# Kernel tuning notes

Measured on AMD Instinct MI355X. Metric: run time of the kernel, lower is better.

The kernel has to match this reference:

```python
import jax, jax.numpy as jnp
from jax import lax
import numpy as np

B, T, F, H = 2048, 256, 64, 32


def setup_inputs() -> dict:
    key = jax.random.key(0)
    k = jax.random.split(key, 7)
    s_ih = 1.0 / np.sqrt(H)  # PyTorch GRU init scale uniform(-1/sqrt(H), 1/sqrt(H))
    return {
        "x": jax.random.normal(k[0], (B, T, F), dtype=jnp.float32),
        "W_ih": jax.random.uniform(k[1], (3 * H, F), minval=-s_ih, maxval=s_ih, dtype=jnp.float32),
        "W_hh": jax.random.uniform(k[2], (3 * H, H), minval=-s_ih, maxval=s_ih, dtype=jnp.float32),
        "b_ih": jax.random.uniform(k[3], (3 * H,), minval=-s_ih, maxval=s_ih, dtype=jnp.float32),
        "b_hh": jax.random.uniform(k[4], (3 * H,), minval=-s_ih, maxval=s_ih, dtype=jnp.float32),
        "W_head": jax.random.uniform(k[5], (1, H), minval=-s_ih, maxval=s_ih, dtype=jnp.float32),
        "b_head": jax.random.uniform(k[6], (1,), minval=-s_ih, maxval=s_ih, dtype=jnp.float32),
    }


def _gru_last_hidden(x, W_ih, W_hh, b_ih, b_hh):
    # Precompute input-to-gate projections for all timesteps: [B,T,3H] -> [T,B,3H]
    xg = jnp.einsum("btf,gf->btg", x, W_ih) + b_ih
    xg = jnp.moveaxis(xg, 1, 0)

    def step(h, xt):
        hg = h @ W_hh.T + b_hh  # [B,3H]
        xr, xz, xn = jnp.split(xt, 3, axis=-1)  # PyTorch gate order: r, z, n
        hr, hz, hn = jnp.split(hg, 3, axis=-1)
        r = jax.nn.sigmoid(xr + hr)
        z = jax.nn.sigmoid(xz + hz)
        n = jnp.tanh(xn + r * hn)
        h_new = (1.0 - z) * n + z * h
        return h_new, None

    h0 = jnp.zeros((x.shape[0], W_hh.shape[1]), dtype=x.dtype)
    hT, _ = lax.scan(step, h0, xg)
    return hT  # [B,H] == out[:, -1, :]


def reference(x, W_ih, W_hh, b_ih, b_hh, W_head, b_head):
    hT = _gru_last_hidden(x, W_ih, W_hh, b_ih, b_hh)
    y = hT @ W_head.T + b_head  # [B,1]
    return jax.nn.sigmoid(y)
```

## Files before the change

kernel.cpp:

```cpp
#include <hip/hip_runtime.h>
#include <cstdint>


#define TSEQ 256
#define CSTRIDE 104

typedef __attribute__((ext_vector_type(8))) short bf16x8;
typedef __attribute__((ext_vector_type(4))) float f32x4;
union BF8 { unsigned u[4]; bf16x8 v; };

__device__ __forceinline__ unsigned bfr(float f) {
    unsigned u = __float_as_uint(f);
    return u + 0x7fffu + ((u >> 16) & 1u);
}
__device__ __forceinline__ unsigned packhi(unsigned a, unsigned b) {
    return __builtin_amdgcn_perm(b, a, 0x07060302u);
}
__device__ __forceinline__ void cvt2(const float4& f0, const float4& f1,
                                     bf16x8& hi, bf16x8& lo) {
    float f[8] = {f0.x,f0.y,f0.z,f0.w, f1.x,f1.y,f1.z,f1.w};
    BF8 H, L;
    #pragma unroll
    for (int d = 0; d < 4; ++d) {
        float a = f[2*d], b = f[2*d+1];
        unsigned ua = __float_as_uint(a), ub = __float_as_uint(b);
        float ra = a - __uint_as_float(ua & 0xffff0000u);
        float rb = b - __uint_as_float(ub & 0xffff0000u);
        H.u[d] = packhi(ua, ub);
        L.u[d] = packhi(bfr(ra), bfr(rb));
    }
    hi = H.v; lo = L.v;
}
__device__ __forceinline__ float sel4(f32x4 v, int u) {
    float a = (u & 1) ? v[1] : v[0];
    float b = (u & 1) ? v[3] : v[2];
    return (u & 2) ? b : a;
}
__device__ __forceinline__ float sigx(float v) {
    return __builtin_amdgcn_rcpf(1.f + exp2f(-1.4426950408889634f * v));
}
__device__ __forceinline__ float tanhx(float v) {
    float e = exp2f(-2.8853900817779268f * fabsf(v));
    return copysignf((1.f - e) * __builtin_amdgcn_rcpf(1.f + e), v);
}

#define MFMA16(A, B, C) __builtin_amdgcn_mfma_f32_16x16x32_bf16((A), (B), (C), 0, 0, 0)

#define QBCAST(x, w) ((unsigned)__builtin_amdgcn_update_dpp( \
        0, (int)(x), ((w) | ((w)<<2) | ((w)<<4) | ((w)<<6)), 0xf, 0xf, true))

__device__ __forceinline__ void barrier_nodrain() {
    asm volatile("s_waitcnt lgkmcnt(0)" ::: "memory");
    __builtin_amdgcn_s_barrier();
    asm volatile("" ::: "memory");
}

__global__ __launch_bounds__(256, 1)
void gru_fused(const float* __restrict__ x, const float* __restrict__ W_ih,
               const float* __restrict__ W_hh, const float* __restrict__ b_ih,
               const float* __restrict__ b_hh, const float* __restrict__ W_head,
               const float* __restrict__ b_head, float* __restrict__ out)
{
    __shared__ float xsh[2][2][16 * CSTRIDE];
    const int tid  = threadIdx.x;
    const int wid  = tid >> 6;
    const int lane = tid & 63;
    const int m = lane & 15, q = lane >> 4;
    const int b0 = blockIdx.x * 8;

    if (wid >= 2) {
        const int pq = wid - 2;
        const int bq = m & 3, u = m >> 2;
        bf16x8 Aih[6][2];
        #pragma unroll
        for (int nt = 0; nt < 6; ++nt)
            #pragma unroll
            for (int c = 0; c < 2; ++c) {
                const float* wp = W_ih + (nt*16 + m)*64 + c*32 + q*8;
                BF8 t;
                #pragma unroll
                for (int d = 0; d < 4; ++d) t.u[d] = packhi(bfr(wp[2*d]), bfr(wp[2*d+1]));
                Aih[nt][c] = t.v;
            }
        float4 ring[4];
        const float* xcol = x + ((size_t)(b0 + pq*4 + bq)*TSEQ + u)*64 + q*8;
        auto ldring = [&](int grp) {
            const float* p = xcol + grp*256;
            ring[0] = ((const float4*)p)[0];        ring[1] = ((const float4*)p)[1];
            ring[2] = ((const float4*)(p+32))[0];   ring[3] = ((const float4*)(p+32))[1];
        };
        auto projwrite = [&](int buf) {
            bf16x8 Xh0, Xl0, Xh1, Xl1;
            cvt2(ring[0], ring[1], Xh0, Xl0);
            cvt2(ring[2], ring[3], Xh1, Xl1);
            #pragma unroll
            for (int nt = 0; nt < 6; ++nt) {
                f32x4 a = MFMA16(Aih[nt][0], Xh0, ((f32x4){0.f,0.f,0.f,0.f}));
                a = MFMA16(Aih[nt][0], Xl0, a);
                a = MFMA16(Aih[nt][1], Xh1, a);
                a = MFMA16(Aih[nt][1], Xl1, a);
                *(f32x4*)&xsh[buf][pq][m*CSTRIDE + nt*16 + q*4] = a;
            }
        };
        ldring(0);
        projwrite(0);
        ldring(1);
        barrier_nodrain();
        for (int g = 0; g < 64; ++g) {
            if (g < 63) {
                projwrite((g + 1) & 1);
                ldring(g + 2 < 64 ? g + 2 : 63);
            }
            barrier_nodrain();
        }
    } else {
        const int cq = wid;
        const int bq = m >> 2, u = m & 3;
        bf16x8 Awh[6];
        #pragma unroll
        for (int nt = 0; nt < 6; ++nt) {
            const float* wp = W_hh + (nt*16 + m)*32;
            BF8 t;
            #pragma unroll
            for (int d = 0; d < 4; ++d) {
                int dd = q*4 + d;
                t.u[d] = packhi(bfr(wp[dd]), bfr(wp[dd + 16]));
            }
            Awh[nt] = t.v;
        }
        f32x4 FRZ[4], BN0, BN1;
        #pragma unroll
        for (int nt = 0; nt < 4; ++nt) {
            f32x4 t;
            #pragma unroll
            for (int r = 0; r < 4; ++r) { int g = nt*16 + q*4 + r; t[r] = b_ih[g] + b_hh[g]; }
            FRZ[nt] = t;
        }
        #pragma unroll
        for (int r = 0; r < 4; ++r) { BN0[r] = b_hh[64+q*4+r]; BN1[r] = b_hh[80+q*4+r]; }
        const float fn0 = b_ih[64 + q*4 + u], fn1 = b_ih[80 + q*4 + u];

        unsigned Hd[4] = {0u, 0u, 0u, 0u};
        float hOL = 0.f, hOH = 0.f;
        barrier_nodrain();

        for (int g = 0; g < 64; ++g) {
            const int cbuf = g & 1;
            float xp[4][6];
            #pragma unroll
            for (int s = 0; s < 4; ++s) {
                const float* rp = &xsh[cbuf][cq][(bq + 4*s)*CSTRIDE + q*4 + u];
                #pragma unroll
                for (int nt = 0; nt < 6; ++nt) xp[s][nt] = rp[nt*16];
            }
            #pragma unroll
            for (int s = 0; s < 4; ++s) {
                BF8 bh; bh.u[0]=Hd[0]; bh.u[1]=Hd[1]; bh.u[2]=Hd[2]; bh.u[3]=Hd[3];
                f32x4 a0 = MFMA16(Awh[0], bh.v, FRZ[0]);
                f32x4 a1 = MFMA16(Awh[1], bh.v, FRZ[1]);
                f32x4 a2 = MFMA16(Awh[2], bh.v, FRZ[2]);
                f32x4 a3 = MFMA16(Awh[3], bh.v, FRZ[3]);
                f32x4 a4 = MFMA16(Awh[4], bh.v, BN0);
                f32x4 a5 = MFMA16(Awh[5], bh.v, BN1);

                float r0 = sigx(xp[s][0] + sel4(a0, u));
                float r1 = sigx(xp[s][1] + sel4(a1, u));
                float z0 = sigx(xp[s][2] + sel4(a2, u));
                float z1 = sigx(xp[s][3] + sel4(a3, u));
                float t0 = tanhx(xp[s][4] + fn0 + r0 * sel4(a4, u));
                float t1 = tanhx(xp[s][5] + fn1 + r1 * sel4(a5, u));
                float hNL = t0 + z0 * (hOL - t0);
                float hNH = t1 + z1 * (hOH - t1);
                hOL = hNL; hOH = hNH;

                unsigned pk = packhi(bfr(hNL), bfr(hNH));
                Hd[0] = QBCAST(pk, 0);
                Hd[1] = QBCAST(pk, 1);
                Hd[2] = QBCAST(pk, 2);
                Hd[3] = QBCAST(pk, 3);
            }
            barrier_nodrain();
        }

        float v = hOL * W_head[q*4 + u] + hOH * W_head[16 + q*4 + u];
        v += __shfl_xor(v, 1, 64);
        v += __shfl_xor(v, 2, 64);
        v += __shfl_xor(v, 16, 64);
        v += __shfl_xor(v, 32, 64);
        if (lane < 16 && (lane & 3) == 0)
            out[b0 + cq*4 + (lane >> 2)] = sigx(v + b_head[0]);
    }
}

extern "C" void kernel_launch(void* const* d_in, const int* in_sizes, int n_in,
                              void* d_out, int out_size, void* d_ws, size_t ws_size,
                              hipStream_t stream)
{
    const float* x      = (const float*)d_in[0];
    const float* W_ih   = (const float*)d_in[1];
    const float* W_hh   = (const float*)d_in[2];
    const float* b_ih   = (const float*)d_in[3];
    const float* b_hh   = (const float*)d_in[4];
    const float* W_head = (const float*)d_in[5];
    const float* b_head = (const float*)d_in[6];
    float* out = (float*)d_out;

    gru_fused<<<256, 256, 0, stream>>>(x, W_ih, W_hh, b_ih, b_hh,
                                       W_head, b_head, out);
}
```

Measured before the change: 239.4 us.

## Merge wave pairs so each wave handles two batch groups with interleaved chains

The block shrinks from four waves to two. One wave now projects inputs for both 4-row batch groups, and one wave runs both recurrence chains, A and B, interleaved in the same loop. The goal is instruction-level parallelism: two independent MFMA/activation dependency chains can hide each other's latency inside one wave, instead of relying on separate waves. The trade-offs are higher register pressure and half as many waves per CU, so less latency hiding comes from wave switching.

```diff
diff --git a/kernel.cpp b/kernel.cpp
--- a/kernel.cpp
+++ b/kernel.cpp
@@ -55,7 +55,7 @@
     asm volatile("" ::: "memory");
 }
 
-__global__ __launch_bounds__(256, 1)
+__global__ __launch_bounds__(128, 1)
 void gru_fused(const float* __restrict__ x, const float* __restrict__ W_ih,
                const float* __restrict__ W_hh, const float* __restrict__ b_ih,
                const float* __restrict__ b_hh, const float* __restrict__ W_head,
@@ -68,8 +68,7 @@
     const int m = lane & 15, q = lane >> 4;
     const int b0 = blockIdx.x * 8;
 
-    if (wid >= 2) {
-        const int pq = wid - 2;
+    if (wid == 1) {
         const int bq = m & 3, u = m >> 2;
         bf16x8 Aih[6][2];
         #pragma unroll
@@ -82,24 +81,38 @@
                 for (int d = 0; d < 4; ++d) t.u[d] = packhi(bfr(wp[2*d]), bfr(wp[2*d+1]));
                 Aih[nt][c] = t.v;
             }
-        float4 ring[4];
-        const float* xcol = x + ((size_t)(b0 + pq*4 + bq)*TSEQ + u)*64 + q*8;
+        float4 ringA[4], ringB[4];
+        const float* xcolA = x + ((size_t)(b0 + bq)*TSEQ + u)*64 + q*8;
+        const float* xcolB = x + ((size_t)(b0 + 4 + bq)*TSEQ + u)*64 + q*8;
         auto ldring = [&](int grp) {
-            const float* p = xcol + grp*256;
-            ring[0] = ((const float4*)p)[0];        ring[1] = ((const float4*)p)[1];
-            ring[2] = ((const float4*)(p+32))[0];   ring[3] = ((const float4*)(p+32))[1];
+            const float* pA = xcolA + grp*256;
+            ringA[0] = ((const float4*)pA)[0];        ringA[1] = ((const float4*)pA)[1];
+            ringA[2] = ((const float4*)(pA+32))[0];   ringA[3] = ((const float4*)(pA+32))[1];
+            const float* pB = xcolB + grp*256;
+            ringB[0] = ((const float4*)pB)[0];        ringB[1] = ((const float4*)pB)[1];
+            ringB[2] = ((const float4*)(pB+32))[0];   ringB[3] = ((const float4*)(pB+32))[1];
         };
         auto projwrite = [&](int buf) {
             bf16x8 Xh0, Xl0, Xh1, Xl1;
-            cvt2(ring[0], ring[1], Xh0, Xl0);
-            cvt2(ring[2], ring[3], Xh1, Xl1);
+            cvt2(ringA[0], ringA[1], Xh0, Xl0);
+            cvt2(ringA[2], ringA[3], Xh1, Xl1);
             #pragma unroll
             for (int nt = 0; nt < 6; ++nt) {
                 f32x4 a = MFMA16(Aih[nt][0], Xh0, ((f32x4){0.f,0.f,0.f,0.f}));
                 a = MFMA16(Aih[nt][0], Xl0, a);
                 a = MFMA16(Aih[nt][1], Xh1, a);
                 a = MFMA16(Aih[nt][1], Xl1, a);
-                *(f32x4*)&xsh[buf][pq][m*CSTRIDE + nt*16 + q*4] = a;
+                *(f32x4*)&xsh[buf][0][m*CSTRIDE + nt*16 + q*4] = a;
+            }
+            cvt2(ringB[0], ringB[1], Xh0, Xl0);
+            cvt2(ringB[2], ringB[3], Xh1, Xl1);
+            #pragma unroll
+            for (int nt = 0; nt < 6; ++nt) {
+                f32x4 a = MFMA16(Aih[nt][0], Xh0, ((f32x4){0.f,0.f,0.f,0.f}));
+                a = MFMA16(Aih[nt][0], Xl0, a);
+                a = MFMA16(Aih[nt][1], Xh1, a);
+                a = MFMA16(Aih[nt][1], Xl1, a);
+                *(f32x4*)&xsh[buf][1][m*CSTRIDE + nt*16 + q*4] = a;
             }
         };
         ldring(0);
@@ -114,7 +127,6 @@
             barrier_nodrain();
         }
     } else {
-        const int cq = wid;
         const int bq = m >> 2, u = m & 3;
         bf16x8 Awh[6];
         #pragma unroll
@@ -140,55 +152,84 @@
         for (int r = 0; r < 4; ++r) { BN0[r] = b_hh[64+q*4+r]; BN1[r] = b_hh[80+q*4+r]; }
         const float fn0 = b_ih[64 + q*4 + u], fn1 = b_ih[80 + q*4 + u];
 
-        unsigned Hd[4] = {0u, 0u, 0u, 0u};
-        float hOL = 0.f, hOH = 0.f;
+        unsigned HdA[4] = {0u,0u,0u,0u}, HdB[4] = {0u,0u,0u,0u};
+        float hAL = 0.f, hAH = 0.f, hBL = 0.f, hBH = 0.f;
         barrier_nodrain();
 
         for (int g = 0; g < 64; ++g) {
             const int cbuf = g & 1;
-            float xp[4][6];
+            float xpA[4][6], xpB[4][6];
             #pragma unroll
             for (int s = 0; s < 4; ++s) {
-                const float* rp = &xsh[cbuf][cq][(bq + 4*s)*CSTRIDE + q*4 + u];
+                const float* rpA = &xsh[cbuf][0][(bq + 4*s)*CSTRIDE + q*4 + u];
+                const float* rpB = &xsh[cbuf][1][(bq + 4*s)*CSTRIDE + q*4 + u];
                 #pragma unroll
-                for (int nt = 0; nt < 6; ++nt) xp[s][nt] = rp[nt*16];
+                for (int nt = 0; nt < 6; ++nt) { xpA[s][nt] = rpA[nt*16]; xpB[s][nt] = rpB[nt*16]; }
             }
             #pragma unroll
             for (int s = 0; s < 4; ++s) {
-                BF8 bh; bh.u[0]=Hd[0]; bh.u[1]=Hd[1]; bh.u[2]=Hd[2]; bh.u[3]=Hd[3];
-                f32x4 a0 = MFMA16(Awh[0], bh.v, FRZ[0]);
-                f32x4 a1 = MFMA16(Awh[1], bh.v, FRZ[1]);
-                f32x4 a2 = MFMA16(Awh[2], bh.v, FRZ[2]);
-                f32x4 a3 = MFMA16(Awh[3], bh.v, FRZ[3]);
-                f32x4 a4 = MFMA16(Awh[4], bh.v, BN0);
-                f32x4 a5 = MFMA16(Awh[5], bh.v, BN1);
-
-                float r0 = sigx(xp[s][0] + sel4(a0, u));
-                float r1 = sigx(xp[s][1] + sel4(a1, u));
-                float z0 = sigx(xp[s][2] + sel4(a2, u));
-                float z1 = sigx(xp[s][3] + sel4(a3, u));
-                float t0 = tanhx(xp[s][4] + fn0 + r0 * sel4(a4, u));
-                float t1 = tanhx(xp[s][5] + fn1 + r1 * sel4(a5, u));
-                float hNL = t0 + z0 * (hOL - t0);
-                float hNH = t1 + z1 * (hOH - t1);
-                hOL = hNL; hOH = hNH;
-
-                unsigned pk = packhi(bfr(hNL), bfr(hNH));
-                Hd[0] = QBCAST(pk, 0);
-                Hd[1] = QBCAST(pk, 1);
-                Hd[2] = QBCAST(pk, 2);
-                Hd[3] = QBCAST(pk, 3);
+                BF8 bhA; bhA.u[0]=HdA[0]; bhA.u[1]=HdA[1]; bhA.u[2]=HdA[2]; bhA.u[3]=HdA[3];
+                f32x4 aA0 = MFMA16(Awh[0], bhA.v, FRZ[0]);
+                f32x4 aA1 = MFMA16(Awh[1], bhA.v, FRZ[1]);
+                f32x4 aA2 = MFMA16(Awh[2], bhA.v, FRZ[2]);
+                f32x4 aA3 = MFMA16(Awh[3], bhA.v, FRZ[3]);
+                f32x4 aA4 = MFMA16(Awh[4], bhA.v, BN0);
+                f32x4 aA5 = MFMA16(Awh[5], bhA.v, BN1);
+                BF8 bhB; bhB.u[0]=HdB[0]; bhB.u[1]=HdB[1]; bhB.u[2]=HdB[2]; bhB.u[3]=HdB[3];
+                f32x4 aB0 = MFMA16(Awh[0], bhB.v, FRZ[0]);
+                f32x4 aB1 = MFMA16(Awh[1], bhB.v, FRZ[1]);
+                f32x4 aB2 = MFMA16(Awh[2], bhB.v, FRZ[2]);
+                f32x4 aB3 = MFMA16(Awh[3], bhB.v, FRZ[3]);
+                f32x4 aB4 = MFMA16(Awh[4], bhB.v, BN0);
+                f32x4 aB5 = MFMA16(Awh[5], bhB.v, BN1);
+
+                {
+                    float r0 = sigx(xpA[s][0] + sel4(aA0, u));
+                    float r1 = sigx(xpA[s][1] + sel4(aA1, u));
+                    float z0 = sigx(xpA[s][2] + sel4(aA2, u));
+                    float z1 = sigx(xpA[s][3] + sel4(aA3, u));
+                    float t0 = tanhx(xpA[s][4] + fn0 + r0 * sel4(aA4, u));
+                    float t1 = tanhx(xpA[s][5] + fn1 + r1 * sel4(aA5, u));
+                    float hNL = t0 + z0 * (hAL - t0);
+                    float hNH = t1 + z1 * (hAH - t1);
+                    hAL = hNL; hAH = hNH;
+                    unsigned pk = packhi(bfr(hNL), bfr(hNH));
+                    HdA[0] = QBCAST(pk, 0);
+                    HdA[1] = QBCAST(pk, 1);
+                    HdA[2] = QBCAST(pk, 2);
+                    HdA[3] = QBCAST(pk, 3);
+                }
+                {
+                    float r0 = sigx(xpB[s][0] + sel4(aB0, u));
+                    float r1 = sigx(xpB[s][1] + sel4(aB1, u));
+                    float z0 = sigx(xpB[s][2] + sel4(aB2, u));
+                    float z1 = sigx(xpB[s][3] + sel4(aB3, u));
+                    float t0 = tanhx(xpB[s][4] + fn0 + r0 * sel4(aB4, u));
+                    float t1 = tanhx(xpB[s][5] + fn1 + r1 * sel4(aB5, u));
+                    float hNL = t0 + z0 * (hBL - t0);
+                    float hNH = t1 + z1 * (hBH - t1);
+                    hBL = hNL; hBH = hNH;
+                    unsigned pk = packhi(bfr(hNL), bfr(hNH));
+                    HdB[0] = QBCAST(pk, 0);
+                    HdB[1] = QBCAST(pk, 1);
+                    HdB[2] = QBCAST(pk, 2);
+                    HdB[3] = QBCAST(pk, 3);
+                }
             }
             barrier_nodrain();
         }
 
-        float v = hOL * W_head[q*4 + u] + hOH * W_head[16 + q*4 + u];
-        v += __shfl_xor(v, 1, 64);
-        v += __shfl_xor(v, 2, 64);
-        v += __shfl_xor(v, 16, 64);
-        v += __shfl_xor(v, 32, 64);
-        if (lane < 16 && (lane & 3) == 0)
-            out[b0 + cq*4 + (lane >> 2)] = sigx(v + b_head[0]);
+        const float w0 = W_head[q*4 + u], w1 = W_head[16 + q*4 + u];
+        float vA = hAL * w0 + hAH * w1;
+        float vB = hBL * w0 + hBH * w1;
+        vA += __shfl_xor(vA, 1, 64);  vB += __shfl_xor(vB, 1, 64);
+        vA += __shfl_xor(vA, 2, 64);  vB += __shfl_xor(vB, 2, 64);
+        vA += __shfl_xor(vA, 16, 64); vB += __shfl_xor(vB, 16, 64);
+        vA += __shfl_xor(vA, 32, 64); vB += __shfl_xor(vB, 32, 64);
+        if (lane < 16 && (lane & 3) == 0) {
+            out[b0 + (lane >> 2)]     = sigx(vA + b_head[0]);
+            out[b0 + 4 + (lane >> 2)] = sigx(vB + b_head[0]);
+        }
     }
 }
 
@@ -205,6 +246,6 @@
     const float* b_head = (const float*)d_in[6];
     float* out = (float*)d_out;
 
-    gru_fused<<<256, 256, 0, stream>>>(x, W_ih, W_hh, b_ih, b_hh,
+    gru_fused<<<256, 128, 0, stream>>>(x, W_ih, W_hh, b_ih, b_hh,
                                        W_head, b_head, out);
 }
```

Result: slower. 300.4 us (+25.5%).

## Replace gate transcendentals with shared-reciprocal rational approximations and fold biases into projection

Applied to the files above, without the earlier changes.

Sigmoid and tanh in the recurrent step are replaced by clamped rational polynomial approximations, with one reciprocal shared across the four sigmoid gates and one across the two tanh gates. Input-side biases are folded into the accumulator init of the input projection MFMAs, so the recurrent MFMAs start from zero. The bf16 packing of the hidden state uses a hardware packed-convert instruction. The aim is to shorten the serial per-timestep latency chain by removing exp and rcp instructions, at the cost of approximation error in the activations and slightly different rounding.

```diff
diff --git a/kernel.cpp b/kernel.cpp
--- a/kernel.cpp
+++ b/kernel.cpp
@@ -36,12 +36,22 @@
     float b = (u & 1) ? v[3] : v[2];
     return (u & 2) ? b : a;
 }
-__device__ __forceinline__ float sigx(float v) {
-    return __builtin_amdgcn_rcpf(1.f + exp2f(-1.4426950408889634f * v));
-}
-__device__ __forceinline__ float tanhx(float v) {
-    float e = exp2f(-2.8853900817779268f * fabsf(v));
-    return copysignf((1.f - e) * __builtin_amdgcn_rcpf(1.f + e), v);
+
+__device__ __forceinline__ void sigr(float x, float& xnum, float& den) {
+    float t = x * x;
+    float n = __builtin_fmaf(__builtin_fmaf(__builtin_fmaf(
+                  2.890625e-8f, t, 4.370629e-5f), t, 8.012821e-3f), t, 0.25f);
+    den     = __builtin_fmaf(__builtin_fmaf(__builtin_fmaf(
+                  3.237500e-6f, t, 1.456879e-3f), t, 0.11538462f), t, 1.0f);
+    xnum = x * n;
+}
+__device__ __forceinline__ void tanr(float x, float& xnum, float& den) {
+    float t = x * x;
+    float n = __builtin_fmaf(__builtin_fmaf(__builtin_fmaf(
+                  7.400300e-6f, t, 2.797203e-3f), t, 0.12820513f), t, 1.0f);
+    den     = __builtin_fmaf(__builtin_fmaf(__builtin_fmaf(
+                  2.071987e-4f, t, 2.331002e-2f), t, 0.46153846f), t, 1.0f);
+    xnum = x * n;
 }
 
 #define MFMA16(A, B, C) __builtin_amdgcn_mfma_f32_16x16x32_bf16((A), (B), (C), 0, 0, 0)
@@ -82,6 +92,17 @@
                 for (int d = 0; d < 4; ++d) t.u[d] = packhi(bfr(wp[2*d]), bfr(wp[2*d+1]));
                 Aih[nt][c] = t.v;
             }
+        f32x4 PC[6];
+        #pragma unroll
+        for (int nt = 0; nt < 6; ++nt) {
+            f32x4 t;
+            #pragma unroll
+            for (int r = 0; r < 4; ++r) {
+                int g = nt*16 + q*4 + r;
+                t[r] = (nt < 4) ? (b_ih[g] + b_hh[g]) : b_ih[g];
+            }
+            PC[nt] = t;
+        }
         float4 ring[4];
         const float* xcol = x + ((size_t)(b0 + pq*4 + bq)*TSEQ + u)*64 + q*8;
         auto ldring = [&](int grp) {
@@ -95,7 +116,7 @@
             cvt2(ring[2], ring[3], Xh1, Xl1);
             #pragma unroll
             for (int nt = 0; nt < 6; ++nt) {
-                f32x4 a = MFMA16(Aih[nt][0], Xh0, ((f32x4){0.f,0.f,0.f,0.f}));
+                f32x4 a = MFMA16(Aih[nt][0], Xh0, PC[nt]);
                 a = MFMA16(Aih[nt][0], Xl0, a);
                 a = MFMA16(Aih[nt][1], Xh1, a);
                 a = MFMA16(Aih[nt][1], Xl1, a);
@@ -128,17 +149,10 @@
             }
             Awh[nt] = t.v;
         }
-        f32x4 FRZ[4], BN0, BN1;
-        #pragma unroll
-        for (int nt = 0; nt < 4; ++nt) {
-            f32x4 t;
-            #pragma unroll
-            for (int r = 0; r < 4; ++r) { int g = nt*16 + q*4 + r; t[r] = b_ih[g] + b_hh[g]; }
-            FRZ[nt] = t;
-        }
+        const f32x4 CZ = {0.f, 0.f, 0.f, 0.f};
+        f32x4 BN0, BN1;
         #pragma unroll
         for (int r = 0; r < 4; ++r) { BN0[r] = b_hh[64+q*4+r]; BN1[r] = b_hh[80+q*4+r]; }
-        const float fn0 = b_ih[64 + q*4 + u], fn1 = b_ih[80 + q*4 + u];
 
         unsigned Hd[4] = {0u, 0u, 0u, 0u};
         float hOL = 0.f, hOH = 0.f;
@@ -156,24 +170,41 @@
             #pragma unroll
             for (int s = 0; s < 4; ++s) {
                 BF8 bh; bh.u[0]=Hd[0]; bh.u[1]=Hd[1]; bh.u[2]=Hd[2]; bh.u[3]=Hd[3];
-                f32x4 a0 = MFMA16(Awh[0], bh.v, FRZ[0]);
-                f32x4 a1 = MFMA16(Awh[1], bh.v, FRZ[1]);
-                f32x4 a2 = MFMA16(Awh[2], bh.v, FRZ[2]);
-                f32x4 a3 = MFMA16(Awh[3], bh.v, FRZ[3]);
+                f32x4 a0 = MFMA16(Awh[0], bh.v, CZ);
+                f32x4 a1 = MFMA16(Awh[1], bh.v, CZ);
+                f32x4 a2 = MFMA16(Awh[2], bh.v, CZ);
+                f32x4 a3 = MFMA16(Awh[3], bh.v, CZ);
                 f32x4 a4 = MFMA16(Awh[4], bh.v, BN0);
                 f32x4 a5 = MFMA16(Awh[5], bh.v, BN1);
 
-                float r0 = sigx(xp[s][0] + sel4(a0, u));
-                float r1 = sigx(xp[s][1] + sel4(a1, u));
-                float z0 = sigx(xp[s][2] + sel4(a2, u));
-                float z1 = sigx(xp[s][3] + sel4(a3, u));
-                float t0 = tanhx(xp[s][4] + fn0 + r0 * sel4(a4, u));
-                float t1 = tanhx(xp[s][5] + fn1 + r1 * sel4(a5, u));
-                float hNL = t0 + z0 * (hOL - t0);
-                float hNH = t1 + z1 * (hOH - t1);
+                float xnr0, dr0, xnr1, dr1, xnz0, dz0, xnz1, dz1;
+                sigr(xp[s][0] + sel4(a0, u), xnr0, dr0);
+                sigr(xp[s][1] + sel4(a1, u), xnr1, dr1);
+                sigr(xp[s][2] + sel4(a2, u), xnz0, dz0);
+                sigr(xp[s][3] + sel4(a3, u), xnz1, dz1);
+                float p01 = dr0 * dr1, p23 = dz0 * dz1;
+                float q4 = __builtin_amdgcn_rcpf(p01 * p23);
+                float qa = q4 * p23, qb = q4 * p01;
+                float r0 = fminf(fmaxf(__builtin_fmaf(xnr0, qa * dr1, 0.5f), 0.f), 1.f);
+                float r1 = fminf(fmaxf(__builtin_fmaf(xnr1, qa * dr0, 0.5f), 0.f), 1.f);
+                float z0 = fminf(fmaxf(__builtin_fmaf(xnz0, qb * dz1, 0.5f), 0.f), 1.f);
+                float z1 = fminf(fmaxf(__builtin_fmaf(xnz1, qb * dz0, 0.5f), 0.f), 1.f);
+
+                float v0 = __builtin_fmaf(r0, sel4(a4, u), xp[s][4]);
+                float v1 = __builtin_fmaf(r1, sel4(a5, u), xp[s][5]);
+                float xnt0, dt0, xnt1, dt1;
+                tanr(v0, xnt0, dt0);
+                tanr(v1, xnt1, dt1);
+                float qt = __builtin_amdgcn_rcpf(dt0 * dt1);
+                float t0 = fminf(fmaxf(xnt0 * (qt * dt1), -1.f), 1.f);
+                float t1 = fminf(fmaxf(xnt1 * (qt * dt0), -1.f), 1.f);
+
+                float hNL = __builtin_fmaf(z0, hOL - t0, t0);
+                float hNH = __builtin_fmaf(z1, hOH - t1, t1);
                 hOL = hNL; hOH = hNH;
 
-                unsigned pk = packhi(bfr(hNL), bfr(hNH));
+                unsigned pk;
+                asm("v_cvt_pk_bf16_f32 %0, %1, %2" : "=v"(pk) : "v"(hNL), "v"(hNH));
                 Hd[0] = QBCAST(pk, 0);
                 Hd[1] = QBCAST(pk, 1);
                 Hd[2] = QBCAST(pk, 2);
@@ -187,8 +218,11 @@
         v += __shfl_xor(v, 2, 64);
         v += __shfl_xor(v, 16, 64);
         v += __shfl_xor(v, 32, 64);
-        if (lane < 16 && (lane & 3) == 0)
-            out[b0 + cq*4 + (lane >> 2)] = sigx(v + b_head[0]);
+        if (lane < 16 && (lane & 3) == 0) {
+            float a = v + b_head[0];
+            float e = __builtin_amdgcn_exp2f(-1.4426950408889634f * a);
+            out[b0 + cq*4 + (lane >> 2)] = __builtin_amdgcn_rcpf(1.f + e);
+        }
     }
 }
 
```

After: 237.3 us. About the same (-0.8%).

## Merge two recurrence waves into one interleaved wave and share reciprocals across gates

Applied to the files above, without the earlier changes.

The two wavefronts that each ran the GRU recurrence for four batch rows are merged into one wavefront that interleaves both independent chains, so the block shrinks from 256 to 192 threads. Interleaving gives the MFMA and transcendental units independent work to fill dependency latency in the serial recurrence. Pairs of sigmoid/tanh denominators now share one reciprocal (1/(d0*d1)), raw exp2 builtins are used, and bf16 packing uses the hardware cvt_pk instruction. The cost is doubled serial work per wave on the critical path and more registers, with slight precision risk from the product reciprocal.

```diff
diff --git a/kernel.cpp b/kernel.cpp
--- a/kernel.cpp
+++ b/kernel.cpp
@@ -36,13 +36,6 @@
     float b = (u & 1) ? v[3] : v[2];
     return (u & 2) ? b : a;
 }
-__device__ __forceinline__ float sigx(float v) {
-    return __builtin_amdgcn_rcpf(1.f + exp2f(-1.4426950408889634f * v));
-}
-__device__ __forceinline__ float tanhx(float v) {
-    float e = exp2f(-2.8853900817779268f * fabsf(v));
-    return copysignf((1.f - e) * __builtin_amdgcn_rcpf(1.f + e), v);
-}
 
 #define MFMA16(A, B, C) __builtin_amdgcn_mfma_f32_16x16x32_bf16((A), (B), (C), 0, 0, 0)
 
@@ -55,7 +48,7 @@
     asm volatile("" ::: "memory");
 }
 
-__global__ __launch_bounds__(256, 1)
+__global__ __launch_bounds__(192, 1)
 void gru_fused(const float* __restrict__ x, const float* __restrict__ W_ih,
                const float* __restrict__ W_hh, const float* __restrict__ b_ih,
                const float* __restrict__ b_hh, const float* __restrict__ W_head,
@@ -68,8 +61,8 @@
     const int m = lane & 15, q = lane >> 4;
     const int b0 = blockIdx.x * 8;
 
-    if (wid >= 2) {
-        const int pq = wid - 2;
+    if (wid >= 1) {
+        const int pq = wid - 1;
         const int bq = m & 3, u = m >> 2;
         bf16x8 Aih[6][2];
         #pragma unroll
@@ -114,7 +107,6 @@
             barrier_nodrain();
         }
     } else {
-        const int cq = wid;
         const int bq = m >> 2, u = m & 3;
         bf16x8 Awh[6];
         #pragma unroll
@@ -140,55 +132,107 @@
         for (int r = 0; r < 4; ++r) { BN0[r] = b_hh[64+q*4+r]; BN1[r] = b_hh[80+q*4+r]; }
         const float fn0 = b_ih[64 + q*4 + u], fn1 = b_ih[80 + q*4 + u];
 
-        unsigned Hd[4] = {0u, 0u, 0u, 0u};
-        float hOL = 0.f, hOH = 0.f;
+        unsigned HdA[4] = {0u,0u,0u,0u}, HdB[4] = {0u,0u,0u,0u};
+        float hAL = 0.f, hAH = 0.f, hBL = 0.f, hBH = 0.f;
         barrier_nodrain();
 
+        const float KS = -1.4426950408889634f;
+        const float KT = -2.8853900817779268f;
         for (int g = 0; g < 64; ++g) {
             const int cbuf = g & 1;
-            float xp[4][6];
+            float xpA[4][6], xpB[4][6];
             #pragma unroll
             for (int s = 0; s < 4; ++s) {
-                const float* rp = &xsh[cbuf][cq][(bq + 4*s)*CSTRIDE + q*4 + u];
+                const float* rpA = &xsh[cbuf][0][(bq + 4*s)*CSTRIDE + q*4 + u];
+                const float* rpB = &xsh[cbuf][1][(bq + 4*s)*CSTRIDE + q*4 + u];
                 #pragma unroll
-                for (int nt = 0; nt < 6; ++nt) xp[s][nt] = rp[nt*16];
+                for (int nt = 0; nt < 6; ++nt) { xpA[s][nt] = rpA[nt*16]; xpB[s][nt] = rpB[nt*16]; }
             }
             #pragma unroll
             for (int s = 0; s < 4; ++s) {
-                BF8 bh; bh.u[0]=Hd[0]; bh.u[1]=Hd[1]; bh.u[2]=Hd[2]; bh.u[3]=Hd[3];
-                f32x4 a0 = MFMA16(Awh[0], bh.v, FRZ[0]);
-                f32x4 a1 = MFMA16(Awh[1], bh.v, FRZ[1]);
-                f32x4 a2 = MFMA16(Awh[2], bh.v, FRZ[2]);
-                f32x4 a3 = MFMA16(Awh[3], bh.v, FRZ[3]);
-                f32x4 a4 = MFMA16(Awh[4], bh.v, BN0);
-                f32x4 a5 = MFMA16(Awh[5], bh.v, BN1);
-
-                float r0 = sigx(xp[s][0] + sel4(a0, u));
-                float r1 = sigx(xp[s][1] + sel4(a1, u));
-                float z0 = sigx(xp[s][2] + sel4(a2, u));
-                float z1 = sigx(xp[s][3] + sel4(a3, u));
-                float t0 = tanhx(xp[s][4] + fn0 + r0 * sel4(a4, u));
-                float t1 = tanhx(xp[s][5] + fn1 + r1 * sel4(a5, u));
-                float hNL = t0 + z0 * (hOL - t0);
-                float hNH = t1 + z1 * (hOH - t1);
-                hOL = hNL; hOH = hNH;
-
-                unsigned pk = packhi(bfr(hNL), bfr(hNH));
-                Hd[0] = QBCAST(pk, 0);
-                Hd[1] = QBCAST(pk, 1);
-                Hd[2] = QBCAST(pk, 2);
-                Hd[3] = QBCAST(pk, 3);
+                BF8 bhA; bhA.u[0]=HdA[0]; bhA.u[1]=HdA[1]; bhA.u[2]=HdA[2]; bhA.u[3]=HdA[3];
+                BF8 bhB; bhB.u[0]=HdB[0]; bhB.u[1]=HdB[1]; bhB.u[2]=HdB[2]; bhB.u[3]=HdB[3];
+                f32x4 aA0 = MFMA16(Awh[0], bhA.v, FRZ[0]);
+                f32x4 aB0 = MFMA16(Awh[0], bhB.v, FRZ[0]);
+                f32x4 aA1 = MFMA16(Awh[1], bhA.v, FRZ[1]);
+                f32x4 aB1 = MFMA16(Awh[1], bhB.v, FRZ[1]);
+                f32x4 aA2 = MFMA16(Awh[2], bhA.v, FRZ[2]);
+                f32x4 aB2 = MFMA16(Awh[2], bhB.v, FRZ[2]);
+                f32x4 aA3 = MFMA16(Awh[3], bhA.v, FRZ[3]);
+                f32x4 aB3 = MFMA16(Awh[3], bhB.v, FRZ[3]);
+                f32x4 aA4 = MFMA16(Awh[4], bhA.v, BN0);
+                f32x4 aB4 = MFMA16(Awh[4], bhB.v, BN0);
+                f32x4 aA5 = MFMA16(Awh[5], bhA.v, BN1);
+                f32x4 aB5 = MFMA16(Awh[5], bhB.v, BN1);
+
+                float erA0 = __builtin_amdgcn_exp2f(KS * (xpA[s][0] + sel4(aA0, u)));
+                float erB0 = __builtin_amdgcn_exp2f(KS * (xpB[s][0] + sel4(aB0, u)));
+                float erA1 = __builtin_amdgcn_exp2f(KS * (xpA[s][1] + sel4(aA1, u)));
+                float erB1 = __builtin_amdgcn_exp2f(KS * (xpB[s][1] + sel4(aB1, u)));
+                float ezA0 = __builtin_amdgcn_exp2f(KS * (xpA[s][2] + sel4(aA2, u)));
+                float ezB0 = __builtin_amdgcn_exp2f(KS * (xpB[s][2] + sel4(aB2, u)));
+                float ezA1 = __builtin_amdgcn_exp2f(KS * (xpA[s][3] + sel4(aA3, u)));
+                float ezB1 = __builtin_amdgcn_exp2f(KS * (xpB[s][3] + sel4(aB3, u)));
+                float drA0 = 1.f + erA0, drA1 = 1.f + erA1;
+                float drB0 = 1.f + erB0, drB1 = 1.f + erB1;
+                float dzA0 = 1.f + ezA0, dzA1 = 1.f + ezA1;
+                float dzB0 = 1.f + ezB0, dzB1 = 1.f + ezB1;
+                float qrA = __builtin_amdgcn_rcpf(drA0 * drA1);
+                float qrB = __builtin_amdgcn_rcpf(drB0 * drB1);
+                float qzA = __builtin_amdgcn_rcpf(dzA0 * dzA1);
+                float qzB = __builtin_amdgcn_rcpf(dzB0 * dzB1);
+                float rA0 = drA1 * qrA, rA1 = drA0 * qrA;
+                float rB0 = drB1 * qrB, rB1 = drB0 * qrB;
+                float zA0 = dzA1 * qzA, zA1 = dzA0 * qzA;
+                float zB0 = dzB1 * qzB, zB1 = dzB0 * qzB;
+                float vA0 = xpA[s][4] + fn0 + rA0 * sel4(aA4, u);
+                float vB0 = xpB[s][4] + fn0 + rB0 * sel4(aB4, u);
+                float vA1 = xpA[s][5] + fn1 + rA1 * sel4(aA5, u);
+                float vB1 = xpB[s][5] + fn1 + rB1 * sel4(aB5, u);
+                float etA0 = __builtin_amdgcn_exp2f(KT * fabsf(vA0));
+                float etB0 = __builtin_amdgcn_exp2f(KT * fabsf(vB0));
+                float etA1 = __builtin_amdgcn_exp2f(KT * fabsf(vA1));
+                float etB1 = __builtin_amdgcn_exp2f(KT * fabsf(vB1));
+                float dtA0 = 1.f + etA0, dtA1 = 1.f + etA1;
+                float dtB0 = 1.f + etB0, dtB1 = 1.f + etB1;
+                float qtA = __builtin_amdgcn_rcpf(dtA0 * dtA1);
+                float qtB = __builtin_amdgcn_rcpf(dtB0 * dtB1);
+                float tA0 = copysignf((1.f - etA0) * dtA1 * qtA, vA0);
+                float tB0 = copysignf((1.f - etB0) * dtB1 * qtB, vB0);
+                float tA1 = copysignf((1.f - etA1) * dtA0 * qtA, vA1);
+                float tB1 = copysignf((1.f - etB1) * dtB0 * qtB, vB1);
+                float hALn = tA0 + zA0 * (hAL - tA0);
+                float hBLn = tB0 + zB0 * (hBL - tB0);
+                float hAHn = tA1 + zA1 * (hAH - tA1);
+                float hBHn = tB1 + zB1 * (hBH - tB1);
+                hAL = hALn; hAH = hAHn; hBL = hBLn; hBH = hBHn;
+
+                unsigned pkA, pkB;
+                asm("v_cvt_pk_bf16_f32 %0, %1, %2" : "=v"(pkA) : "v"(hALn), "v"(hAHn));
+                asm("v_cvt_pk_bf16_f32 %0, %1, %2" : "=v"(pkB) : "v"(hBLn), "v"(hBHn));
+                HdA[0] = QBCAST(pkA, 0);  HdB[0] = QBCAST(pkB, 0);
+                HdA[1] = QBCAST(pkA, 1);  HdB[1] = QBCAST(pkB, 1);
+                HdA[2] = QBCAST(pkA, 2);  HdB[2] = QBCAST(pkB, 2);
+                HdA[3] = QBCAST(pkA, 3);  HdB[3] = QBCAST(pkB, 3);
             }
             barrier_nodrain();
         }
 
-        float v = hOL * W_head[q*4 + u] + hOH * W_head[16 + q*4 + u];
-        v += __shfl_xor(v, 1, 64);
-        v += __shfl_xor(v, 2, 64);
-        v += __shfl_xor(v, 16, 64);
-        v += __shfl_xor(v, 32, 64);
-        if (lane < 16 && (lane & 3) == 0)
-            out[b0 + cq*4 + (lane >> 2)] = sigx(v + b_head[0]);
+        const float w0 = W_head[q*4 + u], w1 = W_head[16 + q*4 + u];
+        float vA = hAL * w0 + hAH * w1;
+        float vB = hBL * w0 + hBH * w1;
+        vA += __shfl_xor(vA, 1, 64);  vB += __shfl_xor(vB, 1, 64);
+        vA += __shfl_xor(vA, 2, 64);  vB += __shfl_xor(vB, 2, 64);
+        vA += __shfl_xor(vA, 16, 64); vB += __shfl_xor(vB, 16, 64);
+        vA += __shfl_xor(vA, 32, 64); vB += __shfl_xor(vB, 32, 64);
+        if (lane < 16 && (lane & 3) == 0) {
+            float aA = vA + b_head[0];
+            float eA = __builtin_amdgcn_exp2f(-1.4426950408889634f * aA);
+            out[b0 + (lane >> 2)] = __builtin_amdgcn_rcpf(1.f + eA);
+            float aB = vB + b_head[0];
+            float eB = __builtin_amdgcn_exp2f(-1.4426950408889634f * aB);
+            out[b0 + 4 + (lane >> 2)] = __builtin_amdgcn_rcpf(1.f + eB);
+        }
     }
 }
 
@@ -205,6 +249,6 @@
     const float* b_head = (const float*)d_in[6];
     float* out = (float*)d_out;
 
-    gru_fused<<<256, 256, 0, stream>>>(x, W_ih, W_hh, b_ih, b_hh,
+    gru_fused<<<256, 192, 0, stream>>>(x, W_ih, W_hh, b_ih, b_hh,
                                        W_head, b_head, out);
 }
```

Result: slower. 264.5 us (+10.5%).
